# Performance work log

Measured on AMD Instinct MI355X. Metric: run time of the kernel, lower is better.

Reference implementation:

```python
import jax, jax.numpy as jnp
import numpy as np

E, A, K = 8192, 128, 512  # parallel_envs, num_agents, passengers per env
P = E * K                 # total passengers (global table rows)


def setup_inputs() -> dict:
    key = jax.random.key(0)
    k1, k2, k3, k4, k5, k6 = jax.random.split(key, 6)
    passengers = jax.random.normal(k1, (P, 11), dtype=jnp.float32)
    # column 0 is the env index of each passenger (used to gather timesteps)
    passengers = passengers.at[:, 0].set(jnp.repeat(jnp.arange(E, dtype=jnp.float32), K))
    accepts = jax.random.bernoulli(k2, 0.5, (E, A))
    picks = jax.random.bernoulli(k3, 0.3, (E, A))
    # env-partitioned global passenger indices: row e targets in [e*K, (e+1)*K)
    local_t = jax.random.randint(k4, (E, A), 0, K, dtype=jnp.int32)
    targets = jnp.arange(E, dtype=jnp.int32)[:, None] * K + local_t
    vectors = jax.random.normal(k5, (E, A, 4), dtype=jnp.float32)
    # give a quarter of agents zero src->dst distance so the pick branch fires
    vectors = vectors.at[:, : A // 4, 2:4].set(vectors[:, : A // 4, 0:2])
    # mark last 8 agent slots per env as invalid (all -100)
    vectors = vectors.at[:, -8:, :].set(-100.0)
    timesteps = jax.random.randint(k6, (E,), 0, 1000, dtype=jnp.int32)
    return {"passengers": passengers, "accepts": accepts, "picks": picks,
            "targets": targets, "vectors": vectors, "timesteps": timesteps}


def _distances(vectors):
    d = jnp.sqrt(((vectors[:, :, 0:2] - vectors[:, :, 2:4]) ** 2).sum(-1))
    return jnp.where((vectors == -100.0).all(-1), jnp.inf, d)


def _dup_mask(t, P):
    # torch: unique(return_inverse, return_counts) -> counts[inverse] > 1 & t != -100
    seg = jnp.where(t >= 0, t, P).ravel()  # -100 -> sentinel bucket P
    counts = jax.ops.segment_sum(jnp.ones(seg.shape, jnp.int32), seg, num_segments=P + 1)
    return (counts[seg].reshape(t.shape) > 1) & (t >= 0)


def reference(passengers, accepts, picks, targets, vectors, timesteps):
    E_, A_ = targets.shape
    P_ = passengers.shape[0]

    distances = _distances(vectors)
    accept_t = jnp.where(accepts, targets, -100)

    def cond(carry):
        t, _ = carry
        return _dup_mask(t, P_).any()

    def body(carry):
        t, d = carry
        dup = _dup_mask(t, P_)
        d = jnp.where(dup, d, jnp.inf)  # cumulative, as in torch
        keep = jnp.arange(A_)[None, :] == jnp.argmin(d, axis=1)[:, None]
        t = jnp.where(dup & ~keep, -100, t)
        return t, d

    accept_t, _ = jax.lax.while_loop(cond, body, (accept_t, distances))

    # scatter accept results into passenger table (at most one agent per passenger now)
    valid = accept_t >= 0
    seg = jnp.where(valid, accept_t, P_).ravel()
    accepted = jax.ops.segment_sum(valid.astype(jnp.int32).ravel(), seg, num_segments=P_ + 1)[:P_] > 0
    agent_ids = jnp.broadcast_to(jnp.arange(A_, dtype=jnp.int32)[None, :], (E_, A_))
    agent_of = jax.ops.segment_max(jnp.where(valid, agent_ids, -100).ravel(), seg, num_segments=P_ + 1)[:P_]
    ts = timesteps[passengers[:, 0].astype(jnp.int32)].astype(passengers.dtype)  # per-passenger timestep

    p = passengers
    p = p.at[:, 6].set(jnp.where(accepted, 1.0, p[:, 6]))
    p = p.at[:, 9].set(jnp.where(accepted, ts, p[:, 9]))
    p = p.at[:, 7].set(jnp.where(accepted, agent_of.astype(p.dtype), p[:, 7]))

    # pick transition: only zero-distance picks succeed
    d2 = _distances(vectors)
    pick_t = jnp.where(picks, targets, -100)
    pd = jnp.where(pick_t >= 0, d2, jnp.inf)
    pick_t = jnp.where(pd < 1e-6, pick_t, -100)
    pvalid = pick_t >= 0
    pseg = jnp.where(pvalid, pick_t, P_).ravel()
    picked = jax.ops.segment_sum(pvalid.astype(jnp.int32).ravel(), pseg, num_segments=P_ + 1)[:P_] > 0
    p = p.at[:, 6].set(jnp.where(picked, 2.0, p[:, 6]))
    p = p.at[:, 10].set(jnp.where(picked, ts, p[:, 10]))
    return p
```

## Files before the change

### kernel.cpp

```cpp
#include <hip/hip_runtime.h>

#define E_ENV  8192
#define A_AG   128
#define K_PASS 512
#define ROW_F  11
#define SLICE_F  (K_PASS * ROW_F)
#define SLICE_V4 (SLICE_F / 4)
#define ITERS    (SLICE_V4 / A_AG)


__device__ __forceinline__ void bar_lds()
{
    asm volatile("s_waitcnt lgkmcnt(0)" ::: "memory");
    __builtin_amdgcn_s_barrier();
    asm volatile("" ::: "memory");
}

__global__ __launch_bounds__(128) void k_fused(
    const float4* __restrict__ pass4,
    const int*    __restrict__ accepts,
    const int*    __restrict__ picks,
    const int*    __restrict__ targets,
    const float4* __restrict__ vectors,
    const int*    __restrict__ timesteps,
    float4*       __restrict__ out4)
{
    __shared__ float4 slice4[SLICE_V4];
    __shared__ int    cnt[K_PASS];
    __shared__ float  swv[2];
    __shared__ int    swi[2];

    const int e   = blockIdx.x;
    const int a   = threadIdx.x;
    const int gid = e * A_AG + a;

    float4 v = vectors[gid];
    const int t    = targets[gid];
    const int acc  = accepts[gid];
    const int pick = picks[gid];

    bool invalid = (v.x == -100.0f) && (v.y == -100.0f) &&
                   (v.z == -100.0f) && (v.w == -100.0f);
    float dx = v.x - v.z, dy = v.y - v.w;
    float d = sqrtf(dx * dx + dy * dy);
    if (invalid) d = INFINITY;

    const int tl = t - e * K_PASS;
    int at = (acc != 0) ? t : -100;

    int mix = t ^ acc ^ pick ^ __float_as_int(d);
    int z;
    asm("v_and_b32 %0, 0, %1" : "=v"(z) : "v"(mix));

    const float4* src = pass4 + (size_t)e * SLICE_V4 + z;
    #pragma unroll
    for (int it = 0; it < ITERS; ++it) {
        const int idx = a + it * A_AG;
        __builtin_amdgcn_global_load_lds(
            (const __attribute__((address_space(1))) void*)(src + idx),
            (__attribute__((address_space(3))) void*)(&slice4[idx]),
            16, 0, 0);
    }

    #pragma unroll
    for (int j = 0; j < K_PASS / A_AG; ++j)
        cnt[a + j * A_AG] = 0;
    bar_lds();

    if (at >= 0) atomicAdd(&cnt[tl], 1);
    bar_lds();

    bool dup = (at >= 0) && (cnt[tl] > 1);
    float bv = dup ? d : INFINITY;
    int   bi = a;

    #pragma unroll
    for (int off = 32; off > 0; off >>= 1) {
        float ov = __shfl_xor(bv, off);
        int   oi = __shfl_xor(bi, off);
        if (ov < bv || (ov == bv && oi < bi)) { bv = ov; bi = oi; }
    }
    int wave = a >> 6;
    if ((a & 63) == 0) { swv[wave] = bv; swi[wave] = bi; }
    bar_lds();
    float v0 = swv[0], v1 = swv[1];
    int   i0 = swi[0], i1 = swi[1];
    int bidx = (v1 < v0 || (v1 == v0 && i1 < i0)) ? i1 : i0;

    int f = (dup && a != bidx) ? -100 : at;

    __syncthreads();

    float* sliceF = (float*)slice4;
    const float tsf = (float)timesteps[e];

    if (f >= 0) {
        sliceF[tl * ROW_F + 6] = 1.0f;
        sliceF[tl * ROW_F + 7] = (float)a;
        sliceF[tl * ROW_F + 9] = tsf;
    }
    bar_lds();
    if ((pick != 0) && d < 1e-6f) {
        sliceF[tl * ROW_F + 6]  = 2.0f;
        sliceF[tl * ROW_F + 10] = tsf;
    }
    bar_lds();

    float4* dst = out4 + (size_t)e * SLICE_V4;
    #pragma unroll
    for (int it = 0; it < ITERS; ++it) {
        const int idx = a + it * A_AG;
        dst[idx] = slice4[idx];
    }
}

extern "C" void kernel_launch(void* const* d_in, const int* in_sizes, int n_in,
                              void* d_out, int out_size, void* d_ws, size_t ws_size,
                              hipStream_t stream)
{
    const float* passengers = (const float*)d_in[0];
    const int*   accepts    = (const int*)d_in[1];
    const int*   picks      = (const int*)d_in[2];
    const int*   targets    = (const int*)d_in[3];
    const float* vectors    = (const float*)d_in[4];
    const int*   timesteps  = (const int*)d_in[5];
    float*       out        = (float*)d_out;

    k_fused<<<E_ENV, A_AG, 0, stream>>>(
        (const float4*)passengers, accepts, picks, targets,
        (const float4*)vectors, timesteps, (float4*)out);
}
```

Measured before the change: 330.8 us.

## Make blocks persistent over several envs with double-buffered LDS prefetch

Each block now handles eight environments instead of one, and the grid shrinks to 1024 blocks. While the current env is processed, the next env's passenger slice and per-agent inputs are staged into a second LDS buffer with async global-to-LDS loads, paced by explicit vmcnt waits. This is meant to hide load latency behind compute and stores, and to amortise block launch cost. In exchange LDS use per block roughly doubles, which lowers occupancy, and correctness depends on the hand-counted vmcnt values.

After: 340.9 us. 3.0% more time.

```diff
diff --git a/kernel.cpp b/kernel.cpp
--- a/kernel.cpp
+++ b/kernel.cpp
@@ -7,7 +7,12 @@
 #define SLICE_F  (K_PASS * ROW_F)
 #define SLICE_V4 (SLICE_F / 4)
 #define ITERS    (SLICE_V4 / A_AG)
+#define GRID_B   1024
+#define NE       (E_ENV / GRID_B)
 
+
+typedef const __attribute__((address_space(1))) void* gp_t;
+typedef __attribute__((address_space(3))) void*       lp_t;
 
 __device__ __forceinline__ void bar_lds()
 {
@@ -25,92 +30,117 @@
     const int*    __restrict__ timesteps,
     float4*       __restrict__ out4)
 {
-    __shared__ float4 slice4[SLICE_V4];
+    __shared__ float4 slice[2][SLICE_V4];
+    __shared__ float4 vbuf[2][A_AG];
+    __shared__ int    tbuf[2][A_AG];
+    __shared__ int    abuf[2][A_AG];
+    __shared__ int    pbuf[2][A_AG];
     __shared__ int    cnt[K_PASS];
     __shared__ float  swv[2];
     __shared__ int    swi[2];
 
-    const int e   = blockIdx.x;
-    const int a   = threadIdx.x;
-    const int gid = e * A_AG + a;
+    const int a  = threadIdx.x;
+    const int e0 = blockIdx.x * NE;
 
-    float4 v = vectors[gid];
-    const int t    = targets[gid];
-    const int acc  = accepts[gid];
-    const int pick = picks[gid];
+    float tsf[NE];
+    #pragma unroll
+    for (int j = 0; j < NE; ++j)
+        tsf[j] = (float)timesteps[e0 + j];
 
-    bool invalid = (v.x == -100.0f) && (v.y == -100.0f) &&
-                   (v.z == -100.0f) && (v.w == -100.0f);
-    float dx = v.x - v.z, dy = v.y - v.w;
-    float d = sqrtf(dx * dx + dy * dy);
-    if (invalid) d = INFINITY;
+    auto STAGE = [&](int env, int bi) {
+        const float4* s4 = pass4 + (size_t)env * SLICE_V4;
+        #pragma unroll
+        for (int it = 0; it < ITERS; ++it) {
+            const int idx = a + it * A_AG;
+            __builtin_amdgcn_global_load_lds((gp_t)(s4 + idx),
+                                             (lp_t)(&slice[bi][idx]), 16, 0, 0);
+        }
+        __builtin_amdgcn_global_load_lds((gp_t)(vectors + (size_t)env * A_AG + a),
+                                         (lp_t)(&vbuf[bi][a]), 16, 0, 0);
+        __builtin_amdgcn_global_load_lds((gp_t)(targets + env * A_AG + a),
+                                         (lp_t)(&tbuf[bi][a]), 4, 0, 0);
+        __builtin_amdgcn_global_load_lds((gp_t)(accepts + env * A_AG + a),
+                                         (lp_t)(&abuf[bi][a]), 4, 0, 0);
+        __builtin_amdgcn_global_load_lds((gp_t)(picks + env * A_AG + a),
+                                         (lp_t)(&pbuf[bi][a]), 4, 0, 0);
+    };
 
-    const int tl = t - e * K_PASS;
-    int at = (acc != 0) ? t : -100;
-
-    int mix = t ^ acc ^ pick ^ __float_as_int(d);
-    int z;
-    asm("v_and_b32 %0, 0, %1" : "=v"(z) : "v"(mix));
-
-    const float4* src = pass4 + (size_t)e * SLICE_V4 + z;
-    #pragma unroll
-    for (int it = 0; it < ITERS; ++it) {
-        const int idx = a + it * A_AG;
-        __builtin_amdgcn_global_load_lds(
-            (const __attribute__((address_space(1))) void*)(src + idx),
-            (__attribute__((address_space(3))) void*)(&slice4[idx]),
-            16, 0, 0);
-    }
+    STAGE(e0, 0);
 
     #pragma unroll
-    for (int j = 0; j < K_PASS / A_AG; ++j)
-        cnt[a + j * A_AG] = 0;
-    bar_lds();
+    for (int j = 0; j < NE; ++j) {
+        const int cur = j & 1;
+        const int e   = e0 + j;
 
-    if (at >= 0) atomicAdd(&cnt[tl], 1);
-    bar_lds();
+        if (j + 1 < NE) STAGE(e + 1, cur ^ 1);
 
-    bool dup = (at >= 0) && (cnt[tl] > 1);
-    float bv = dup ? d : INFINITY;
-    int   bi = a;
+        if (j == 0)          asm volatile("s_waitcnt vmcnt(15)" ::: "memory");
+        else if (j + 1 < NE) asm volatile("s_waitcnt vmcnt(26)" ::: "memory");
+        else                 asm volatile("s_waitcnt vmcnt(11)" ::: "memory");
+        __builtin_amdgcn_s_barrier();
+        asm volatile("" ::: "memory");
 
-    #pragma unroll
-    for (int off = 32; off > 0; off >>= 1) {
-        float ov = __shfl_xor(bv, off);
-        int   oi = __shfl_xor(bi, off);
-        if (ov < bv || (ov == bv && oi < bi)) { bv = ov; bi = oi; }
-    }
-    int wave = a >> 6;
-    if ((a & 63) == 0) { swv[wave] = bv; swi[wave] = bi; }
-    bar_lds();
-    float v0 = swv[0], v1 = swv[1];
-    int   i0 = swi[0], i1 = swi[1];
-    int bidx = (v1 < v0 || (v1 == v0 && i1 < i0)) ? i1 : i0;
+        float4 v  = vbuf[cur][a];
+        int   t   = tbuf[cur][a];
+        int   acc = abuf[cur][a];
+        int   pk  = pbuf[cur][a];
 
-    int f = (dup && a != bidx) ? -100 : at;
+        bool invalid = (v.x == -100.0f) && (v.y == -100.0f) &&
+                       (v.z == -100.0f) && (v.w == -100.0f);
+        float dx = v.x - v.z, dy = v.y - v.w;
+        float d = sqrtf(dx * dx + dy * dy);
+        if (invalid) d = INFINITY;
 
-    __syncthreads();
+        const int tl = t - e * K_PASS;
+        int at = (acc != 0) ? t : -100;
 
-    float* sliceF = (float*)slice4;
-    const float tsf = (float)timesteps[e];
+        #pragma unroll
+        for (int jj = 0; jj < K_PASS / A_AG; ++jj)
+            cnt[a + jj * A_AG] = 0;
+        bar_lds();
 
-    if (f >= 0) {
-        sliceF[tl * ROW_F + 6] = 1.0f;
-        sliceF[tl * ROW_F + 7] = (float)a;
-        sliceF[tl * ROW_F + 9] = tsf;
-    }
-    bar_lds();
-    if ((pick != 0) && d < 1e-6f) {
-        sliceF[tl * ROW_F + 6]  = 2.0f;
-        sliceF[tl * ROW_F + 10] = tsf;
-    }
-    bar_lds();
+        if (at >= 0) atomicAdd(&cnt[tl], 1);
+        bar_lds();
 
-    float4* dst = out4 + (size_t)e * SLICE_V4;
-    #pragma unroll
-    for (int it = 0; it < ITERS; ++it) {
-        const int idx = a + it * A_AG;
-        dst[idx] = slice4[idx];
+        bool dup = (at >= 0) && (cnt[tl] > 1);
+        float bv = dup ? d : INFINITY;
+        int   bi = a;
+        #pragma unroll
+        for (int off = 32; off > 0; off >>= 1) {
+            float ov = __shfl_xor(bv, off);
+            int   oi = __shfl_xor(bi, off);
+            if (ov < bv || (ov == bv && oi < bi)) { bv = ov; bi = oi; }
+        }
+        int wave = a >> 6;
+        if ((a & 63) == 0) { swv[wave] = bv; swi[wave] = bi; }
+        bar_lds();
+        float v0 = swv[0], v1 = swv[1];
+        int   i0 = swi[0], i1 = swi[1];
+        int bidx = (v1 < v0 || (v1 == v0 && i1 < i0)) ? i1 : i0;
+
+        int f = (dup && a != bidx) ? -100 : at;
+
+        float* sf = (float*)&slice[cur][0];
+        if (f >= 0) {
+            sf[tl * ROW_F + 6] = 1.0f;
+            sf[tl * ROW_F + 7] = (float)a;
+            sf[tl * ROW_F + 9] = tsf[j];
+        }
+        bar_lds();
+        if ((pk != 0) && d < 1e-6f) {
+            sf[tl * ROW_F + 6]  = 2.0f;
+            sf[tl * ROW_F + 10] = tsf[j];
+        }
+        bar_lds();
+
+        float4* dst = out4 + (size_t)e * SLICE_V4;
+        #pragma unroll
+        for (int it = 0; it < ITERS; ++it) {
+            const int idx = a + it * A_AG;
+            dst[idx] = slice[cur][idx];
+        }
+
+        bar_lds();
     }
 }
 
@@ -126,7 +156,7 @@
     const int*   timesteps  = (const int*)d_in[5];
     float*       out        = (float*)d_out;
 
-    k_fused<<<E_ENV, A_AG, 0, stream>>>(
+    k_fused<<<GRID_B, A_AG, 0, stream>>>(
         (const float4*)passengers, accepts, picks, targets,
         (const float4*)vectors, timesteps, (float4*)out);
 }
```
